# Performance work log

Measured on AMD Instinct MI355X. Metric: run time of the kernel, lower is better.

The kernel has to match this reference:

```python
import jax, jax.numpy as jnp
import numpy as np
from jax import lax

MAXV = 8      # convex intersection of two quads has at most 8 vertices
EPS = 1e-7
LOSS_WEIGHT = 1.0


def _edge_cross(A, B, P):
    # z of (B-A) x (P-A); >= 0 means P is on the left of directed edge A->B (inside for CCW poly)
    return (B[0] - A[0]) * (P[1] - A[1]) - (B[1] - A[1]) * (P[0] - A[0])


def _clip_halfplane(pts, n, A, B):
    # Sutherland-Hodgman clip of polygon pts[:n] against left halfplane of edge A->B.
    # pts: (MAXV,2) buffer, n: traced vertex count. Returns new buffer + count.
    def body(i, carry):
        out, m = carry
        valid = i < n
        cur = pts[i]
        nxt = pts[jnp.mod(i + 1, jnp.maximum(n, 1))]
        dc = _edge_cross(A, B, cur)
        dn = _edge_cross(A, B, nxt)
        denom = dc - dn
        t = dc / jnp.where(jnp.abs(denom) < EPS, 1.0, denom)
        ip = cur + t * (nxt - cur)
        add_cur = valid & (dc >= 0)
        idx = jnp.minimum(m, MAXV - 1)
        out = jnp.where(add_cur, out.at[idx].set(cur), out)
        m = m + add_cur.astype(jnp.int32)
        add_ip = valid & jnp.logical_xor(dc >= 0, dn >= 0)
        idx = jnp.minimum(m, MAXV - 1)
        out = jnp.where(add_ip, out.at[idx].set(ip), out)
        m = m + add_ip.astype(jnp.int32)
        return out, m
    out0 = jnp.zeros((MAXV, 2), pts.dtype)
    return lax.fori_loop(0, MAXV, body, (out0, jnp.int32(0)))


def _shoelace_masked(pts, n):
    # signed area of pts[:n] (fixed-size loop, masked)
    def body(i, acc):
        valid = i < n
        cur = pts[i]
        nxt = pts[jnp.mod(i + 1, jnp.maximum(n, 1))]
        term = cur[0] * nxt[1] - cur[1] * nxt[0]
        return acc + jnp.where(valid, term, jnp.zeros((), pts.dtype))
    return 0.5 * lax.fori_loop(0, MAXV, body, jnp.zeros((), pts.dtype))


def _quad_signed_area(p):  # p: (4,2)
    x, y = p[:, 0], p[:, 1]
    return 0.5 * jnp.sum(x * jnp.roll(y, -1) - y * jnp.roll(x, -1))


def _diou_single(p, t):
    # p, t: (4,2) quads -> scalar poly DIoU loss (a=0 => standard DIoU penalty)
    sa_p = _quad_signed_area(p)
    sa_t = _quad_signed_area(t)
    p = jnp.where(sa_p < 0, p[::-1], p)   # force CCW orientation
    t = jnp.where(sa_t < 0, t[::-1], t)
    area_p = jnp.abs(sa_p)
    area_t = jnp.abs(sa_t)
    # clip p by the 4 halfplanes of t
    buf = jnp.zeros((MAXV, 2), p.dtype).at[:4].set(p)
    n = jnp.int32(4)
    for k in range(4):
        buf, n = _clip_halfplane(buf, n, t[k], t[(k + 1) % 4])
    inter = jnp.abs(_shoelace_masked(buf, n))
    union = area_p + area_t - inter
    iou = inter / (union + EPS)
    cp = p.mean(0)
    ct = t.mean(0)
    d2 = jnp.sum((cp - ct) ** 2)
    allp = jnp.concatenate([p, t], axis=0)
    c2 = jnp.sum((allp.max(0) - allp.min(0)) ** 2) + EPS
    return 1.0 - iou + d2 / c2


def setup_inputs() -> dict:
    key = jax.random.key(0)
    k1, k2 = jax.random.split(key)
    N = 2_000_000
    pred = jax.random.uniform(k1, (N, 8), dtype=jnp.float32)
    target = jax.random.uniform(k2, (N, 8), dtype=jnp.float32)
    return {"pred": pred, "target": target}


def reference(pred, target):
    p = pred.reshape(-1, 4, 2)
    t = target.reshape(-1, 4, 2)
    losses = jax.vmap(_diou_single)(p, t)  # (N,)
    return LOSS_WEIGHT * losses.mean()
```

## Files before the change

### kernel.cpp

```cpp
#include <hip/hip_runtime.h>

#define NBLOCKS 2048
#define NTHREADS 256
#define FEPS 1e-7f

__device__ __forceinline__ float frcp(float x) { return __builtin_amdgcn_rcpf(x); }

__device__ __forceinline__ int clip1_to_lds(float2* base,
                                            const float (&px)[4], const float (&py)[4],
                                            float ex, float ey, float h) {
    float c[4];
#pragma unroll
    for (int j = 0; j < 4; ++j)
        c[j] = fmaf(ex, py[j], -fmaf(ey, px[j], h));
    int m = 0;
#pragma unroll
    for (int i = 0; i < 4; ++i) {
        const int ip1 = (i + 1) & 3;
        float dc = c[i], dn = c[ip1];
        float nx = px[ip1], ny = py[ip1];
        float denom = dc - dn;
        float d = (fabsf(denom) < FEPS) ? 1.0f : denom;
        float t = dc * frcp(d);
        float ipx = fmaf(t, nx - px[i], px[i]);
        float ipy = fmaf(t, ny - py[i], py[i]);
        bool sc = dc >= 0.0f, sn = dn >= 0.0f;

        bool add_cur = sc;
        int i1 = add_cur ? m : 8;
        base[i1 * NTHREADS] = make_float2(px[i], py[i]);
        m += add_cur;

        bool add_ip = (sc != sn);
        int i2 = add_ip ? m : 8;
        base[i2 * NTHREADS] = make_float2(ipx, ipy);
        m += add_ip;
    }
    return m;
}

__device__ __forceinline__ int clip_lds(float2* base, int n,
                                        float ex, float ey, float h) {
    float vx[8], vy[8], c[8];
#pragma unroll
    for (int j = 0; j < 8; ++j) {
        float2 v = base[j * NTHREADS];
        vx[j] = v.x; vy[j] = v.y;
        c[j] = fmaf(ex, vy[j], -fmaf(ey, vx[j], h));
    }
    int m = 0;
#pragma unroll
    for (int i = 0; i < 8; ++i) {
        if (i >= 4 && !__any(i < n)) break;
        bool valid = i < n;
        bool wrap = (i + 1 == n);
        const int ip1 = (i < 7) ? (i + 1) : 7;
        float nx = wrap ? vx[0] : vx[ip1];
        float ny = wrap ? vy[0] : vy[ip1];
        float dc = c[i];
        float dn = wrap ? c[0] : c[ip1];
        float denom = dc - dn;
        float d = (fabsf(denom) < FEPS) ? 1.0f : denom;
        float t = dc * frcp(d);
        float ipx = fmaf(t, nx - vx[i], vx[i]);
        float ipy = fmaf(t, ny - vy[i], vy[i]);
        bool sc = dc >= 0.0f, sn = dn >= 0.0f;

        bool add_cur = valid && sc;
        int i1;
        if (i < 4) i1 = add_cur ? m : 8;
        else       i1 = add_cur ? ((m < 7) ? m : 7) : 8;
        base[i1 * NTHREADS] = make_float2(vx[i], vy[i]);
        m += add_cur;

        bool add_ip = valid && (sc != sn);
        int i2;
        if (i < 4) i2 = add_ip ? m : 8;
        else       i2 = add_ip ? ((m < 7) ? m : 7) : 8;
        base[i2 * NTHREADS] = make_float2(ipx, ipy);
        m += add_ip;
    }
    return m;
}

__device__ __forceinline__ float diou_quad(float2* base,
                                           float4 pa, float4 pb, float4 ta, float4 tb) {
    float px[4] = {pa.x, pa.z, pb.x, pb.z};
    float py[4] = {pa.y, pa.w, pb.y, pb.w};
    float tx[4] = {ta.x, ta.z, tb.x, tb.z};
    float ty[4] = {ta.y, ta.w, tb.y, tb.w};

    float sa_p = 0.5f * ((px[0] * py[1] - py[0] * px[1]) +
                         (px[1] * py[2] - py[1] * px[2]) +
                         (px[2] * py[3] - py[2] * px[3]) +
                         (px[3] * py[0] - py[3] * px[0]));
    float sa_t = 0.5f * ((tx[0] * ty[1] - ty[0] * tx[1]) +
                         (tx[1] * ty[2] - ty[1] * tx[2]) +
                         (tx[2] * ty[3] - ty[2] * tx[3]) +
                         (tx[3] * ty[0] - ty[3] * tx[0]));

    if (sa_p < 0.0f) {
        float t0;
        t0 = px[0]; px[0] = px[3]; px[3] = t0;
        t0 = px[1]; px[1] = px[2]; px[2] = t0;
        t0 = py[0]; py[0] = py[3]; py[3] = t0;
        t0 = py[1]; py[1] = py[2]; py[2] = t0;
    }
    if (sa_t < 0.0f) {
        float t0;
        t0 = tx[0]; tx[0] = tx[3]; tx[3] = t0;
        t0 = tx[1]; tx[1] = tx[2]; tx[2] = t0;
        t0 = ty[0]; ty[0] = ty[3]; ty[3] = t0;
        t0 = ty[1]; ty[1] = ty[2]; ty[2] = t0;
    }
    float area_p = fabsf(sa_p);
    float area_t = fabsf(sa_t);

    int n;
    {
        float ex = tx[1] - tx[0], ey = ty[1] - ty[0];
        n = clip1_to_lds(base, px, py, ex, ey, fmaf(ex, ty[0], -ey * tx[0]));
    }
    {
        float ex = tx[2] - tx[1], ey = ty[2] - ty[1];
        n = clip_lds(base, n, ex, ey, fmaf(ex, ty[1], -ey * tx[1]));
    }
    {
        float ex = tx[3] - tx[2], ey = ty[3] - ty[2];
        n = clip_lds(base, n, ex, ey, fmaf(ex, ty[2], -ey * tx[2]));
    }
    {
        float ex = tx[0] - tx[3], ey = ty[0] - ty[3];
        n = clip_lds(base, n, ex, ey, fmaf(ex, ty[3], -ey * tx[3]));
    }

    float vx[8], vy[8];
#pragma unroll
    for (int j = 0; j < 8; ++j) {
        float2 v = base[j * NTHREADS];
        vx[j] = v.x; vy[j] = v.y;
    }
    float acc = 0.0f;
#pragma unroll
    for (int i = 0; i < 8; ++i) {
        if (i >= 4 && !__any(i < n)) break;
        bool valid = i < n;
        bool wrap = (i + 1 == n);
        const int ip1 = (i < 7) ? (i + 1) : 7;
        float nx = wrap ? vx[0] : vx[ip1];
        float ny = wrap ? vy[0] : vy[ip1];
        float term = vx[i] * ny - vy[i] * nx;
        acc += valid ? term : 0.0f;
    }
    float inter = fabsf(0.5f * acc);
    float uni = area_p + area_t - inter;
    float iou = inter * frcp(uni + FEPS);

    float cpx = 0.25f * (px[0] + px[1] + px[2] + px[3]);
    float cpy = 0.25f * (py[0] + py[1] + py[2] + py[3]);
    float ctx = 0.25f * (tx[0] + tx[1] + tx[2] + tx[3]);
    float cty = 0.25f * (ty[0] + ty[1] + ty[2] + ty[3]);
    float d2 = (cpx - ctx) * (cpx - ctx) + (cpy - cty) * (cpy - cty);

    float minx = fminf(fminf(fminf(px[0], px[1]), fminf(px[2], px[3])),
                       fminf(fminf(tx[0], tx[1]), fminf(tx[2], tx[3])));
    float maxx = fmaxf(fmaxf(fmaxf(px[0], px[1]), fmaxf(px[2], px[3])),
                       fmaxf(fmaxf(tx[0], tx[1]), fmaxf(tx[2], tx[3])));
    float miny = fminf(fminf(fminf(py[0], py[1]), fminf(py[2], py[3])),
                       fminf(fminf(ty[0], ty[1]), fminf(ty[2], ty[3])));
    float maxy = fmaxf(fmaxf(fmaxf(py[0], py[1]), fmaxf(py[2], py[3])),
                       fmaxf(fmaxf(ty[0], ty[1]), fmaxf(ty[2], ty[3])));
    float c2 = (maxx - minx) * (maxx - minx) + (maxy - miny) * (maxy - miny) + FEPS;

    return 1.0f - iou + d2 * frcp(c2);
}

__global__ __launch_bounds__(NTHREADS, 4) void diou_main(const float* __restrict__ pred,
                                                         const float* __restrict__ target,
                                                         double* __restrict__ partial,
                                                         int N) {
    __shared__ float2 poly[9 * NTHREADS];
    __shared__ double wsum[NTHREADS / 64];
    float2* base = &poly[threadIdx.x];

    const float4* p4 = reinterpret_cast<const float4*>(pred);
    const float4* t4 = reinterpret_cast<const float4*>(target);

    double acc = 0.0;
    for (int i = blockIdx.x * NTHREADS + threadIdx.x; i < N; i += NBLOCKS * NTHREADS) {
        float4 pa = p4[2 * i], pb = p4[2 * i + 1];
        float4 ta = t4[2 * i], tb = t4[2 * i + 1];
        acc += (double)diou_quad(base, pa, pb, ta, tb);
    }

#pragma unroll
    for (int off = 32; off > 0; off >>= 1) acc += __shfl_down(acc, off, 64);
    int lane = threadIdx.x & 63, wid = threadIdx.x >> 6;
    if (lane == 0) wsum[wid] = acc;
    __syncthreads();
    if (threadIdx.x == 0) {
        double s = 0.0;
#pragma unroll
        for (int w = 0; w < NTHREADS / 64; ++w) s += wsum[w];
        partial[blockIdx.x] = s;
    }
}

__global__ __launch_bounds__(256) void diou_finalize(const double* __restrict__ partial,
                                                     float* __restrict__ out,
                                                     int nparts, double invN) {
    __shared__ double s[256];
    double acc = 0.0;
    for (int i = threadIdx.x; i < nparts; i += 256) acc += partial[i];
    s[threadIdx.x] = acc;
    __syncthreads();
#pragma unroll
    for (int off = 128; off > 0; off >>= 1) {
        if (threadIdx.x < off) s[threadIdx.x] += s[threadIdx.x + off];
        __syncthreads();
    }
    if (threadIdx.x == 0) out[0] = (float)(s[0] * invN);
}

extern "C" void kernel_launch(void* const* d_in, const int* in_sizes, int n_in,
                              void* d_out, int out_size, void* d_ws, size_t ws_size,
                              hipStream_t stream) {
    const float* pred = (const float*)d_in[0];
    const float* target = (const float*)d_in[1];
    float* out = (float*)d_out;
    int N = in_sizes[0] / 8;

    double* partial = (double*)d_ws;

    diou_main<<<NBLOCKS, NTHREADS, 0, stream>>>(pred, target, partial, N);
    diou_finalize<<<1, 256, 0, stream>>>(partial, out, NBLOCKS, 1.0 / (double)N);
}
```

Measured before the change: 50.21 us.

## Interleave two independent quad pairs per thread for ILP and drop wave-vote early exits

Each thread now processes two elements (i and i+half) per iteration, interleaving their clip passes using two separate LDS polygon buffers. The goal is more instruction-level parallelism to hide LDS and reciprocal latency. The __any early-exit branches are removed, the quad signed area uses the diagonal cross-product form, and the centroid and bbox terms are precomputed in setup. In exchange it doubles LDS use per block and raises register pressure, which may lower occupancy.

```diff
diff --git a/kernel.cpp b/kernel.cpp
--- a/kernel.cpp
+++ b/kernel.cpp
@@ -5,42 +5,106 @@
 #define FEPS 1e-7f
 
 __device__ __forceinline__ float frcp(float x) { return __builtin_amdgcn_rcpf(x); }
-
-__device__ __forceinline__ int clip1_to_lds(float2* base,
-                                            const float (&px)[4], const float (&py)[4],
-                                            float ex, float ey, float h) {
+__device__ __forceinline__ float fmin3(float a, float b, float c) { return fminf(fminf(a, b), c); }
+__device__ __forceinline__ float fmax3(float a, float b, float c) { return fmaxf(fmaxf(a, b), c); }
+
+struct Quad {
+    float px[4], py[4];
+    float tx[4], ty[4];
+    float area_p, area_t;
+    float d2c2;
+};
+
+__device__ __forceinline__ void setup(Quad& q,
+                                      float4 pa, float4 pb, float4 ta, float4 tb) {
+    q.px[0] = pa.x; q.py[0] = pa.y; q.px[1] = pa.z; q.py[1] = pa.w;
+    q.px[2] = pb.x; q.py[2] = pb.y; q.px[3] = pb.z; q.py[3] = pb.w;
+    q.tx[0] = ta.x; q.ty[0] = ta.y; q.tx[1] = ta.z; q.ty[1] = ta.w;
+    q.tx[2] = tb.x; q.ty[2] = tb.y; q.tx[3] = tb.z; q.ty[3] = tb.w;
+
+    float sp = 0.5f * ((q.px[0] - q.px[2]) * (q.py[1] - q.py[3]) -
+                       (q.px[1] - q.px[3]) * (q.py[0] - q.py[2]));
+    float st = 0.5f * ((q.tx[0] - q.tx[2]) * (q.ty[1] - q.ty[3]) -
+                       (q.tx[1] - q.tx[3]) * (q.ty[0] - q.ty[2]));
+
+    if (sp < 0.0f) {
+        float w;
+        w = q.px[0]; q.px[0] = q.px[3]; q.px[3] = w;
+        w = q.px[1]; q.px[1] = q.px[2]; q.px[2] = w;
+        w = q.py[0]; q.py[0] = q.py[3]; q.py[3] = w;
+        w = q.py[1]; q.py[1] = q.py[2]; q.py[2] = w;
+    }
+    if (st < 0.0f) {
+        float w;
+        w = q.tx[0]; q.tx[0] = q.tx[3]; q.tx[3] = w;
+        w = q.tx[1]; q.tx[1] = q.tx[2]; q.tx[2] = w;
+        w = q.ty[0]; q.ty[0] = q.ty[3]; q.ty[3] = w;
+        w = q.ty[1]; q.ty[1] = q.ty[2]; q.ty[2] = w;
+    }
+    q.area_p = fabsf(sp);
+    q.area_t = fabsf(st);
+
+    float cpx = 0.25f * (q.px[0] + q.px[1] + q.px[2] + q.px[3]);
+    float cpy = 0.25f * (q.py[0] + q.py[1] + q.py[2] + q.py[3]);
+    float ctx = 0.25f * (q.tx[0] + q.tx[1] + q.tx[2] + q.tx[3]);
+    float cty = 0.25f * (q.ty[0] + q.ty[1] + q.ty[2] + q.ty[3]);
+    float dx = cpx - ctx, dy = cpy - cty;
+    float d2 = dx * dx + dy * dy;
+
+    float minx = fmin3(fmin3(q.px[0], q.px[1], q.px[2]),
+                       fmin3(q.px[3], q.tx[0], q.tx[1]),
+                       fminf(q.tx[2], q.tx[3]));
+    float maxx = fmax3(fmax3(q.px[0], q.px[1], q.px[2]),
+                       fmax3(q.px[3], q.tx[0], q.tx[1]),
+                       fmaxf(q.tx[2], q.tx[3]));
+    float miny = fmin3(fmin3(q.py[0], q.py[1], q.py[2]),
+                       fmin3(q.py[3], q.ty[0], q.ty[1]),
+                       fminf(q.ty[2], q.ty[3]));
+    float maxy = fmax3(fmax3(q.py[0], q.py[1], q.py[2]),
+                       fmax3(q.py[3], q.ty[0], q.ty[1]),
+                       fmaxf(q.ty[2], q.ty[3]));
+    float bx = maxx - minx, by = maxy - miny;
+    float c2 = bx * bx + by * by + FEPS;
+    q.d2c2 = d2 * frcp(c2);
+}
+
+__device__ __forceinline__ int clip1_to_lds(float2* base, const Quad& q) {
+    float ex = q.tx[1] - q.tx[0], ey = q.ty[1] - q.ty[0];
+    float h = fmaf(ex, q.ty[0], -ey * q.tx[0]);
     float c[4];
 #pragma unroll
     for (int j = 0; j < 4; ++j)
-        c[j] = fmaf(ex, py[j], -fmaf(ey, px[j], h));
+        c[j] = fmaf(ex, q.py[j], -fmaf(ey, q.px[j], h));
     int m = 0;
 #pragma unroll
     for (int i = 0; i < 4; ++i) {
         const int ip1 = (i + 1) & 3;
         float dc = c[i], dn = c[ip1];
-        float nx = px[ip1], ny = py[ip1];
         float denom = dc - dn;
         float d = (fabsf(denom) < FEPS) ? 1.0f : denom;
         float t = dc * frcp(d);
-        float ipx = fmaf(t, nx - px[i], px[i]);
-        float ipy = fmaf(t, ny - py[i], py[i]);
+        float ipx = fmaf(t, q.px[ip1] - q.px[i], q.px[i]);
+        float ipy = fmaf(t, q.py[ip1] - q.py[i], q.py[i]);
         bool sc = dc >= 0.0f, sn = dn >= 0.0f;
 
-        bool add_cur = sc;
-        int i1 = add_cur ? m : 8;
-        base[i1 * NTHREADS] = make_float2(px[i], py[i]);
-        m += add_cur;
-
-        bool add_ip = (sc != sn);
-        int i2 = add_ip ? m : 8;
+        int i1 = sc ? m : 8;
+        base[i1 * NTHREADS] = make_float2(q.px[i], q.py[i]);
+        m += sc;
+
+        bool aip = (sc != sn);
+        int i2 = aip ? m : 8;
         base[i2 * NTHREADS] = make_float2(ipx, ipy);
-        m += add_ip;
+        m += aip;
     }
     return m;
 }
 
-__device__ __forceinline__ int clip_lds(float2* base, int n,
-                                        float ex, float ey, float h) {
+template <int K>
+__device__ __forceinline__ int clip_pass(float2* base, int n, const Quad& q) {
+    constexpr int K1 = (K + 1) & 3;
+    float ex = q.tx[K1] - q.tx[K], ey = q.ty[K1] - q.ty[K];
+    float h = fmaf(ex, q.ty[K], -ey * q.tx[K]);
+
     float vx[8], vy[8], c[8];
 #pragma unroll
     for (int j = 0; j < 8; ++j) {
@@ -51,7 +115,6 @@
     int m = 0;
 #pragma unroll
     for (int i = 0; i < 8; ++i) {
-        if (i >= 4 && !__any(i < n)) break;
         bool valid = i < n;
         bool wrap = (i + 1 == n);
         const int ip1 = (i < 7) ? (i + 1) : 7;
@@ -83,57 +146,7 @@
     return m;
 }
 
-__device__ __forceinline__ float diou_quad(float2* base,
-                                           float4 pa, float4 pb, float4 ta, float4 tb) {
-    float px[4] = {pa.x, pa.z, pb.x, pb.z};
-    float py[4] = {pa.y, pa.w, pb.y, pb.w};
-    float tx[4] = {ta.x, ta.z, tb.x, tb.z};
-    float ty[4] = {ta.y, ta.w, tb.y, tb.w};
-
-    float sa_p = 0.5f * ((px[0] * py[1] - py[0] * px[1]) +
-                         (px[1] * py[2] - py[1] * px[2]) +
-                         (px[2] * py[3] - py[2] * px[3]) +
-                         (px[3] * py[0] - py[3] * px[0]));
-    float sa_t = 0.5f * ((tx[0] * ty[1] - ty[0] * tx[1]) +
-                         (tx[1] * ty[2] - ty[1] * tx[2]) +
-                         (tx[2] * ty[3] - ty[2] * tx[3]) +
-                         (tx[3] * ty[0] - ty[3] * tx[0]));
-
-    if (sa_p < 0.0f) {
-        float t0;
-        t0 = px[0]; px[0] = px[3]; px[3] = t0;
-        t0 = px[1]; px[1] = px[2]; px[2] = t0;
-        t0 = py[0]; py[0] = py[3]; py[3] = t0;
-        t0 = py[1]; py[1] = py[2]; py[2] = t0;
-    }
-    if (sa_t < 0.0f) {
-        float t0;
-        t0 = tx[0]; tx[0] = tx[3]; tx[3] = t0;
-        t0 = tx[1]; tx[1] = tx[2]; tx[2] = t0;
-        t0 = ty[0]; ty[0] = ty[3]; ty[3] = t0;
-        t0 = ty[1]; ty[1] = ty[2]; ty[2] = t0;
-    }
-    float area_p = fabsf(sa_p);
-    float area_t = fabsf(sa_t);
-
-    int n;
-    {
-        float ex = tx[1] - tx[0], ey = ty[1] - ty[0];
-        n = clip1_to_lds(base, px, py, ex, ey, fmaf(ex, ty[0], -ey * tx[0]));
-    }
-    {
-        float ex = tx[2] - tx[1], ey = ty[2] - ty[1];
-        n = clip_lds(base, n, ex, ey, fmaf(ex, ty[1], -ey * tx[1]));
-    }
-    {
-        float ex = tx[3] - tx[2], ey = ty[3] - ty[2];
-        n = clip_lds(base, n, ex, ey, fmaf(ex, ty[2], -ey * tx[2]));
-    }
-    {
-        float ex = tx[0] - tx[3], ey = ty[0] - ty[3];
-        n = clip_lds(base, n, ex, ey, fmaf(ex, ty[3], -ey * tx[3]));
-    }
-
+__device__ __forceinline__ float shoelace(const float2* base, int n) {
     float vx[8], vy[8];
 #pragma unroll
     for (int j = 0; j < 8; ++j) {
@@ -143,7 +156,6 @@
     float acc = 0.0f;
 #pragma unroll
     for (int i = 0; i < 8; ++i) {
-        if (i >= 4 && !__any(i < n)) break;
         bool valid = i < n;
         bool wrap = (i + 1 == n);
         const int ip1 = (i < 7) ? (i + 1) : 7;
@@ -152,45 +164,67 @@
         float term = vx[i] * ny - vy[i] * nx;
         acc += valid ? term : 0.0f;
     }
-    float inter = fabsf(0.5f * acc);
-    float uni = area_p + area_t - inter;
+    return acc;
+}
+
+__device__ __forceinline__ float finish(const Quad& q, float sl) {
+    float inter = fabsf(0.5f * sl);
+    float uni = q.area_p + q.area_t - inter;
     float iou = inter * frcp(uni + FEPS);
-
-    float cpx = 0.25f * (px[0] + px[1] + px[2] + px[3]);
-    float cpy = 0.25f * (py[0] + py[1] + py[2] + py[3]);
-    float ctx = 0.25f * (tx[0] + tx[1] + tx[2] + tx[3]);
-    float cty = 0.25f * (ty[0] + ty[1] + ty[2] + ty[3]);
-    float d2 = (cpx - ctx) * (cpx - ctx) + (cpy - cty) * (cpy - cty);
-
-    float minx = fminf(fminf(fminf(px[0], px[1]), fminf(px[2], px[3])),
-                       fminf(fminf(tx[0], tx[1]), fminf(tx[2], tx[3])));
-    float maxx = fmaxf(fmaxf(fmaxf(px[0], px[1]), fmaxf(px[2], px[3])),
-                       fmaxf(fmaxf(tx[0], tx[1]), fmaxf(tx[2], tx[3])));
-    float miny = fminf(fminf(fminf(py[0], py[1]), fminf(py[2], py[3])),
-                       fminf(fminf(ty[0], ty[1]), fminf(ty[2], ty[3])));
-    float maxy = fmaxf(fmaxf(fmaxf(py[0], py[1]), fmaxf(py[2], py[3])),
-                       fmaxf(fmaxf(ty[0], ty[1]), fmaxf(ty[2], ty[3])));
-    float c2 = (maxx - minx) * (maxx - minx) + (maxy - miny) * (maxy - miny) + FEPS;
-
-    return 1.0f - iou + d2 * frcp(c2);
+    return 1.0f - iou + q.d2c2;
+}
+
+__device__ __forceinline__ float diou_one(float2* base,
+                                          float4 pa, float4 pb, float4 ta, float4 tb) {
+    Quad q;
+    setup(q, pa, pb, ta, tb);
+    int n = clip1_to_lds(base, q);
+    n = clip_pass<1>(base, n, q);
+    n = clip_pass<2>(base, n, q);
+    n = clip_pass<3>(base, n, q);
+    return finish(q, shoelace(base, n));
 }
 
 __global__ __launch_bounds__(NTHREADS, 4) void diou_main(const float* __restrict__ pred,
                                                          const float* __restrict__ target,
                                                          double* __restrict__ partial,
                                                          int N) {
-    __shared__ float2 poly[9 * NTHREADS];
+    __shared__ float2 poly[18 * NTHREADS];
     __shared__ double wsum[NTHREADS / 64];
-    float2* base = &poly[threadIdx.x];
+    float2* baseA = &poly[threadIdx.x];
+    float2* baseB = baseA + 9 * NTHREADS;
 
     const float4* p4 = reinterpret_cast<const float4*>(pred);
     const float4* t4 = reinterpret_cast<const float4*>(target);
 
+    const int half = N >> 1;
     double acc = 0.0;
-    for (int i = blockIdx.x * NTHREADS + threadIdx.x; i < N; i += NBLOCKS * NTHREADS) {
-        float4 pa = p4[2 * i], pb = p4[2 * i + 1];
-        float4 ta = t4[2 * i], tb = t4[2 * i + 1];
-        acc += (double)diou_quad(base, pa, pb, ta, tb);
+    for (int p = blockIdx.x * NTHREADS + threadIdx.x; p < half; p += NBLOCKS * NTHREADS) {
+        const int iB = p + half;
+        float4 paA = p4[2 * p], pbA = p4[2 * p + 1];
+        float4 taA = t4[2 * p], tbA = t4[2 * p + 1];
+        float4 paB = p4[2 * iB], pbB = p4[2 * iB + 1];
+        float4 taB = t4[2 * iB], tbB = t4[2 * iB + 1];
+
+        Quad A, B;
+        setup(A, paA, pbA, taA, tbA);
+        setup(B, paB, pbB, taB, tbB);
+        int nA = clip1_to_lds(baseA, A);
+        int nB = clip1_to_lds(baseB, B);
+        nA = clip_pass<1>(baseA, nA, A);
+        nB = clip_pass<1>(baseB, nB, B);
+        nA = clip_pass<2>(baseA, nA, A);
+        nB = clip_pass<2>(baseB, nB, B);
+        nA = clip_pass<3>(baseA, nA, A);
+        nB = clip_pass<3>(baseB, nB, B);
+        float slA = shoelace(baseA, nA);
+        float slB = shoelace(baseB, nB);
+        acc += (double)finish(A, slA) + (double)finish(B, slB);
+    }
+    if ((N & 1) && blockIdx.x == 0 && threadIdx.x == 0) {
+        const int last = N - 1;
+        acc += (double)diou_one(baseA, p4[2 * last], p4[2 * last + 1],
+                                t4[2 * last], t4[2 * last + 1]);
     }
 
 #pragma unroll
```

Result: slower. 59.23 us (+18.0%).
